# Performance work log

Hardware: AMD Instinct MI355X
Metric: run time of the kernel (lower is better)

The kernel has to match this reference:

```python
import jax, jax.numpy as jnp
import numpy as np
import jax.scipy.linalg

BATCH = 1048576
M_NUM = 2
DT = 0.0166667
NN_RATIO = 0.5
SLOPE = 0.01  # torch LeakyReLU default negative_slope


def setup_inputs() -> dict:
    key = jax.random.key(0)
    ks = jax.random.split(key, 16)
    inp = {}
    inp["SS"] = jax.random.normal(ks[0], (BATCH, 2), dtype=jnp.float32)
    inp["Alphas"] = jax.random.uniform(ks[1], (BATCH, M_NUM), dtype=jnp.float32)
    # per-muscle scalar parameters (positive so sqrt(K*I) is valid)
    inp["K0s"] = jax.random.uniform(ks[2], (M_NUM,), minval=0.5, maxval=1.5)
    inp["K1s"] = jax.random.uniform(ks[3], (M_NUM,), minval=0.5, maxval=1.5)
    inp["L0s"] = jax.random.uniform(ks[4], (M_NUM,), minval=0.5, maxval=1.5)
    inp["L1s"] = jax.random.uniform(ks[5], (M_NUM,), minval=0.1, maxval=0.6)
    inp["Ms"] = jnp.array([1.0, -1.0], dtype=jnp.float32)  # moment arms
    inp["I_p"] = jnp.array([1.0], dtype=jnp.float32)
    inp["B_p"] = jnp.array([0.05], dtype=jnp.float32)
    inp["K_p"] = jnp.array([1.0], dtype=jnp.float32)
    # per-muscle compensational MLP weights: 3-32-32-32-1 (eval mode, dropout off)
    s = 0.1
    inp["W1"] = jax.random.normal(ks[6], (M_NUM, 3, 32)) * s
    inp["b1"] = jax.random.normal(ks[7], (M_NUM, 32)) * s
    inp["W2"] = jax.random.normal(ks[8], (M_NUM, 32, 32)) * s
    inp["b2"] = jax.random.normal(ks[9], (M_NUM, 32)) * s
    inp["W3"] = jax.random.normal(ks[10], (M_NUM, 32, 32)) * s
    inp["b3"] = jax.random.normal(ks[11], (M_NUM, 32)) * s
    inp["W4"] = jax.random.normal(ks[12], (M_NUM, 32, 1)) * s
    inp["b4"] = jax.random.normal(ks[13], (M_NUM, 1)) * s
    return inp


def _leaky(x):
    return jnp.where(x >= 0, x, SLOPE * x)


def reference(SS, Alphas, K0s, K1s, L0s, L1s, Ms, I_p, B_p, K_p,
              W1, b1, W2, b2, W3, b3, W4, b4):
    B = SS.shape[0]
    a = jnp.clip(Alphas, 0.0, 1.0)                      # (B, m)
    # muscle length / speed via scalar moment arms
    l = SS[:, 0:1] * Ms[None, :]                        # (B, m)
    dl = SS[:, 1:2] * Ms[None, :]                       # (B, m)
    # compensational MLPs, vectorized over muscles
    x = jnp.stack([l, dl, a], axis=-1)                  # (B, m, 3)
    h = _leaky(jnp.einsum('bmi,mio->bmo', x, W1) + b1[None])
    h = _leaky(jnp.einsum('bmi,mio->bmo', h, W2) + b2[None])
    h = _leaky(jnp.einsum('bmi,mio->bmo', h, W3) + b3[None])
    nn_out = jnp.tanh(jnp.einsum('bmi,mio->bmo', h, W4) + b4[None])[..., 0] * NN_RATIO  # (B, m)

    I0, B0p, K0p = I_p[0], B_p[0], K_p[0]
    K_m = K0s[None, :] + K1s[None, :] * a               # (B, m)
    K_tot = jnp.sum(K_m * Ms[None, :] ** 2, axis=1)     # (B,)
    A10 = -(K_tot + K0p) / I0
    D = 2.0 * jnp.sqrt(K_tot * I0)
    A11 = -(D + B0p) / I0
    B_F = K_m * (L0s[None, :] + L1s[None, :] * a - jnp.abs(l)) \
        + K1s[None, :] * L1s[None, :] * a * a * nn_out   # (B, m)
    B10 = jnp.sum(B_F * Ms[None, :], axis=1) / I0       # (B,)

    # Build block matrix M6 = [[A*dt, B*dt, 0], [0, 0, I2], [0, 0, 0]]
    M6 = jnp.zeros((B, 6, 6), dtype=SS.dtype)
    M6 = M6.at[:, 0, 1].set(DT)
    M6 = M6.at[:, 1, 0].set(A10 * DT)
    M6 = M6.at[:, 1, 1].set(A11 * DT)
    M6 = M6.at[:, 1, 2].set(B10 * DT)
    M6 = M6.at[:, 1, 3].set(DT / I0)
    M6 = M6.at[:, 2, 4].set(1.0)
    M6 = M6.at[:, 3, 5].set(1.0)

    expMT = jax.vmap(jax.scipy.linalg.expm)(M6)         # (B, 6, 6)
    Ad = expMT[:, :2, :2]
    Bd1 = expMT[:, :2, 4:6]
    Bd0 = expMT[:, :2, 2:4] - Bd1
    u = jnp.array([1.0, 0.0], dtype=SS.dtype)           # U0 = U1 = [1, 0]
    SSout = (jnp.einsum('bij,bj->bi', Ad, SS)
             + jnp.einsum('bij,j->bi', Bd0, u)
             + jnp.einsum('bij,j->bi', Bd1, u))          # (B, 2)
    return SSout[:, :1], SSout
```

## Files before the change

### kernel.cpp

```cpp
#include <hip/hip_runtime.h>
#include <hip/hip_bf16.h>

#define NTHREADS 512
#define WAVES    8
#define NBLOCKS  768
#define DT_F     0.0166667f

typedef _Float16 f16x4 __attribute__((ext_vector_type(4)));
typedef _Float16 f16x2 __attribute__((ext_vector_type(2)));
typedef float    f32x4 __attribute__((ext_vector_type(4)));

#define BF16_PROBE 0xBF803F80u

#define OW1 0
#define OB1 192
#define OW2 256
#define OB2 2368
#define OW3 2432
#define OB3 4544
#define OW4 4608
#define OB4 4672
#define SMEM_F 4680

__device__ __forceinline__ float leaky(float x) { return fmaxf(x, 0.01f * x); }

__device__ __forceinline__ float tanh_fast(float x) {
    const float xc = fminf(fmaxf(x, -10.0f), 10.0f);
    const float t  = __expf(2.0f * xc);
    return (t - 1.0f) * __builtin_amdgcn_rcpf(t + 1.0f);
}

__device__ __forceinline__ f16x2 pkrtz(float a, float b) {
    return __builtin_bit_cast(f16x2, __builtin_amdgcn_cvt_pkrtz(a, b));
}

__device__ __forceinline__ f16x4 leaky_cvt(const f32x4 D) {
    f16x2 lo = pkrtz(D[0], D[1]);
    f16x2 hi = pkrtz(D[2], D[3]);
    const f16x2 sl = {(_Float16)0.01f, (_Float16)0.01f};
    lo = __builtin_elementwise_max(lo, lo * sl);
    hi = __builtin_elementwise_max(hi, hi * sl);
    return __builtin_shufflevector(lo, hi, 0, 1, 2, 3);
}

__device__ __forceinline__ void epilogue_math(
    const float* P, float ss0, float ss1, float a0, float a1,
    float nn0, float nn1, float& o0f, float& o1f)
{
    const float K00 = P[0], K01 = P[1], K10 = P[2], K11 = P[3];
    const float L00 = P[4], L01 = P[5], L10 = P[6], L11 = P[7];
    const float Ms0 = P[8], Ms1 = P[9];
    const float I0  = P[10], B0p = P[11], K0p = P[12];

    const float Km0   = fmaf(K10, a0, K00);
    const float Km1   = fmaf(K11, a1, K01);
    const float K_tot = Km0*Ms0*Ms0 + Km1*Ms1*Ms1;
    const float invI  = 1.0f / I0;
    const float A10   = -(K_tot + K0p) * invI;
    const float Dd    = 2.0f * sqrtf(K_tot * I0);
    const float A11   = -(Dd + B0p) * invI;
    const float absl0 = fabsf(ss0 * Ms0);
    const float absl1 = fabsf(ss0 * Ms1);
    const float BF0   = Km0 * (L00 + L10*a0 - absl0) + K10*L10*a0*a0*nn0;
    const float BF1   = Km1 * (L01 + L11*a1 - absl1) + K11*L11*a1*a1*nn1;
    const float B10   = (BF0*Ms0 + BF1*Ms1) * invI;

    const float t01 = DT_F;
    const float t10 = A10 * DT_F;
    const float t11 = A11 * DT_F;

    float p00 = 1.0f/120.0f, p01 = 0.0f, p10 = 0.0f, p11 = 1.0f/120.0f;
    const float coef[4] = {1.0f/24.0f, 1.0f/6.0f, 0.5f, 1.0f};
    #pragma unroll
    for (int j = 0; j < 4; ++j) {
        const float cj  = coef[j];
        const float n00 = p01*t10 + cj;
        const float n01 = p00*t01 + p01*t11;
        const float n10 = p11*t10;
        const float n11 = p10*t01 + p11*t11 + cj;
        p00 = n00; p01 = n01; p10 = n10; p11 = n11;
    }
    const float e00 = 1.0f + t01*p10;
    const float e01 = t01*p11;
    const float e10 = t10*p00 + t11*p10;
    const float e11 = 1.0f + t10*p01 + t11*p11;

    const float cscale = DT_F * B10;
    o0f = fmaf(e00, ss0, fmaf(e01, ss1, p01 * cscale));
    o1f = fmaf(e10, ss0, fmaf(e11, ss1, p11 * cscale));
}

__device__ __forceinline__ float ldb(const __hip_bfloat16* p, int i) {
    return __bfloat162float(p[i]);
}

__device__ void run_bf16_fallback(
    const void* SSv, const void* ALv, const void* K0sv, const void* K1sv,
    const void* L0sv, const void* L1sv, const void* Msv, const void* I_pv,
    const void* B_pv, const void* K_pv, const void* W1v, const void* b1v,
    const void* W2v, const void* b2v, const void* W3v, const void* b3v,
    const void* W4v, const void* b4v, void* outv, int batch)
{
    const __hip_bfloat16* SS = (const __hip_bfloat16*)SSv;
    const __hip_bfloat16* AL = (const __hip_bfloat16*)ALv;
    const __hip_bfloat16* W1 = (const __hip_bfloat16*)W1v;
    const __hip_bfloat16* b1 = (const __hip_bfloat16*)b1v;
    const __hip_bfloat16* W2 = (const __hip_bfloat16*)W2v;
    const __hip_bfloat16* b2 = (const __hip_bfloat16*)b2v;
    const __hip_bfloat16* W3 = (const __hip_bfloat16*)W3v;
    const __hip_bfloat16* b3 = (const __hip_bfloat16*)b3v;
    const __hip_bfloat16* W4 = (const __hip_bfloat16*)W4v;
    const __hip_bfloat16* b4 = (const __hip_bfloat16*)b4v;

    float P[13];
    P[0] = ldb((const __hip_bfloat16*)K0sv, 0); P[1] = ldb((const __hip_bfloat16*)K0sv, 1);
    P[2] = ldb((const __hip_bfloat16*)K1sv, 0); P[3] = ldb((const __hip_bfloat16*)K1sv, 1);
    P[4] = ldb((const __hip_bfloat16*)L0sv, 0); P[5] = ldb((const __hip_bfloat16*)L0sv, 1);
    P[6] = ldb((const __hip_bfloat16*)L1sv, 0); P[7] = ldb((const __hip_bfloat16*)L1sv, 1);
    P[8] = ldb((const __hip_bfloat16*)Msv, 0);  P[9] = ldb((const __hip_bfloat16*)Msv, 1);
    P[10] = ldb((const __hip_bfloat16*)I_pv, 0);
    P[11] = ldb((const __hip_bfloat16*)B_pv, 0);
    P[12] = ldb((const __hip_bfloat16*)K_pv, 0);

    const int stride = gridDim.x * blockDim.x;
    for (int e = blockIdx.x * blockDim.x + threadIdx.x; e < batch; e += stride) {
        const float ss0 = ldb(SS, 2*e), ss1 = ldb(SS, 2*e+1);
        float a0 = fminf(fmaxf(ldb(AL, 2*e),   0.0f), 1.0f);
        float a1 = fminf(fmaxf(ldb(AL, 2*e+1), 0.0f), 1.0f);
        float nn[2];
        #pragma unroll 1
        for (int m = 0; m < 2; ++m) {
            const float am = m ? a1 : a0;
            const float l = ss0 * P[8+m], dl = ss1 * P[8+m];
            float h[32];
            #pragma unroll
            for (int o = 0; o < 32; ++o)
                h[o] = leaky(fmaf(l, ldb(W1, m*96+o),
                             fmaf(dl, ldb(W1, m*96+32+o),
                             fmaf(am, ldb(W1, m*96+64+o), ldb(b1, m*32+o)))));
            float g[32];
            #pragma unroll 1
            for (int oc = 0; oc < 4; ++oc) {
                float acc[8];
                #pragma unroll
                for (int j = 0; j < 8; ++j) acc[j] = ldb(b2, m*32+oc*8+j);
                #pragma unroll
                for (int k = 0; k < 32; ++k) {
                    #pragma unroll
                    for (int j = 0; j < 8; ++j)
                        acc[j] = fmaf(h[k], ldb(W2, m*1024+k*32+oc*8+j), acc[j]);
                }
                #pragma unroll
                for (int j = 0; j < 8; ++j) g[oc*8+j] = leaky(acc[j]);
            }
            float h3[32];
            #pragma unroll 1
            for (int oc = 0; oc < 4; ++oc) {
                float acc[8];
                #pragma unroll
                for (int j = 0; j < 8; ++j) acc[j] = ldb(b3, m*32+oc*8+j);
                #pragma unroll
                for (int k = 0; k < 32; ++k) {
                    #pragma unroll
                    for (int j = 0; j < 8; ++j)
                        acc[j] = fmaf(g[k], ldb(W3, m*1024+k*32+oc*8+j), acc[j]);
                }
                #pragma unroll
                for (int j = 0; j < 8; ++j) h3[oc*8+j] = leaky(acc[j]);
            }
            float acc = ldb(b4, m);
            #pragma unroll
            for (int k = 0; k < 32; ++k) acc = fmaf(h3[k], ldb(W4, m*32+k), acc);
            nn[m] = tanh_fast(acc) * 0.5f;
        }
        float o0f, o1f;
        epilogue_math(P, ss0, ss1, a0, a1, nn[0], nn[1], o0f, o1f);
        __hip_bfloat16* out0 = (__hip_bfloat16*)outv;
        __hip_bfloat162* out1 = (__hip_bfloat162*)(out0 + batch);
        out0[e] = __float2bfloat16(o0f);
        __hip_bfloat162 pr;
        pr.x = __float2bfloat16(o0f);
        pr.y = __float2bfloat16(o1f);
        out1[e] = pr;
    }
}

__global__ __launch_bounds__(NTHREADS) void joint_kernel(
    const void* __restrict__ SSv, const void* __restrict__ ALv,
    const void* __restrict__ K0sv, const void* __restrict__ K1sv,
    const void* __restrict__ L0sv, const void* __restrict__ L1sv,
    const void* __restrict__ Msv,  const void* __restrict__ I_pv,
    const void* __restrict__ B_pv, const void* __restrict__ K_pv,
    const void* __restrict__ W1v,  const void* __restrict__ b1v,
    const void* __restrict__ W2v,  const void* __restrict__ b2v,
    const void* __restrict__ W3v,  const void* __restrict__ b3v,
    const void* __restrict__ W4v,  const void* __restrict__ b4v,
    void* __restrict__ outv, int batch)
{
    const unsigned probe = *(const unsigned*)Msv;
    if (probe == BF16_PROBE) {
        run_bf16_fallback(SSv, ALv, K0sv, K1sv, L0sv, L1sv, Msv, I_pv, B_pv,
                          K_pv, W1v, b1v, W2v, b2v, W3v, b3v, W4v, b4v,
                          outv, batch);
        return;
    }

    const float* SS = (const float*)SSv;
    const float* AL = (const float*)ALv;
    const float* W1 = (const float*)W1v;  const float* b1 = (const float*)b1v;
    const float* W2 = (const float*)W2v;  const float* b2 = (const float*)b2v;
    const float* W3 = (const float*)W3v;  const float* b3 = (const float*)b3v;
    const float* W4 = (const float*)W4v;  const float* b4 = (const float*)b4v;

    const int tid  = threadIdx.x;
    const int wave = tid >> 6;
    const int lane = tid & 63;
    const int n    = lane & 15;
    const int q    = lane >> 4;

    __shared__ __align__(16) float sm[SMEM_F];
    for (int i = tid; i < 192;  i += NTHREADS) sm[OW1+i] = W1[i];
    for (int i = tid; i < 2048; i += NTHREADS) {
        const int mi = i >> 10, rem = i & 1023, in = rem >> 5, out = rem & 31;
        sm[OW2 + mi*1056 + in*33 + out] = W2[i];
        sm[OW3 + mi*1056 + in*33 + out] = W3[i];
    }
    for (int i = tid; i < 64;   i += NTHREADS) {
        sm[OB1+i] = b1[i]; sm[OB2+i] = b2[i];
        sm[OB3+i] = b3[i]; sm[OW4+i] = W4[i];
    }
    if (tid < 2) sm[OB4+tid] = b4[tid];
    __syncthreads();

    f16x4 A1[2][2];
    #pragma unroll
    for (int mi = 0; mi < 2; ++mi)
        #pragma unroll
        for (int i = 0; i < 2; ++i)
            #pragma unroll
            for (int j = 0; j < 4; ++j) {
                const int k = q*4 + j;
                float v = 0.0f;
                if (k < 3)       v = sm[OW1 + mi*96 + k*32 + i*16 + n];
                else if (k == 3) v = sm[OB1 + mi*32 + i*16 + n];
                A1[mi][i][j] = (_Float16)v;
            }
    f16x4 A2[2][2][2], A3[2][2][2];
    #pragma unroll
    for (int mi = 0; mi < 2; ++mi)
        #pragma unroll
        for (int i = 0; i < 2; ++i)
            #pragma unroll
            for (int kb = 0; kb < 2; ++kb)
                #pragma unroll
                for (int j = 0; j < 4; ++j) {
                    const int in = kb*16 + q*4 + j;
                    A2[mi][i][kb][j] = (_Float16)sm[OW2 + mi*1056 + in*33 + i*16 + n];
                    A3[mi][i][kb][j] = (_Float16)sm[OW3 + mi*1056 + in*33 + i*16 + n];
                }
    f16x4 A4[2][2];
    #pragma unroll
    for (int mi = 0; mi < 2; ++mi)
        #pragma unroll
        for (int kb = 0; kb < 2; ++kb)
            #pragma unroll
            for (int j = 0; j < 4; ++j)
                A4[mi][kb][j] = (_Float16)sm[OW4 + mi*32 + kb*16 + q*4 + j];
    f32x4 Cb2[2][2], Cb3[2][2];
    #pragma unroll
    for (int mi = 0; mi < 2; ++mi) {
        #pragma unroll
        for (int i = 0; i < 2; ++i) {
            Cb2[mi][i] = *(const f32x4*)&sm[OB2 + mi*32 + i*16 + q*4];
            Cb3[mi][i] = *(const f32x4*)&sm[OB3 + mi*32 + i*16 + q*4];
        }
    }
    const float b4s0 = sm[OB4], b4s1 = sm[OB4+1];

    float P[13];
    P[0]  = ((const float*)K0sv)[0]; P[1]  = ((const float*)K0sv)[1];
    P[2]  = ((const float*)K1sv)[0]; P[3]  = ((const float*)K1sv)[1];
    P[4]  = ((const float*)L0sv)[0]; P[5]  = ((const float*)L0sv)[1];
    P[6]  = ((const float*)L1sv)[0]; P[7]  = ((const float*)L1sv)[1];
    P[8]  = ((const float*)Msv)[0];  P[9]  = ((const float*)Msv)[1];
    P[10] = ((const float*)I_pv)[0];
    P[11] = ((const float*)B_pv)[0];
    P[12] = ((const float*)K_pv)[0];

    const f32x4 zero = {0.0f, 0.0f, 0.0f, 0.0f};
    const int nGroups    = (batch + 63) >> 6;
    const int waveId     = blockIdx.x * WAVES + wave;
    const int waveStride = gridDim.x * WAVES;

    #pragma unroll 1
    for (int grp = waveId; grp < nGroups; grp += waveStride) {
        const int ebase = grp * 64;
        float my_r0 = 0.0f, my_r1 = 0.0f;

        #pragma unroll 1
        for (int p = 0; p < 2; ++p) {
            float2 s[2];
            float a0c[2], a1c[2];
            #pragma unroll
            for (int ti = 0; ti < 2; ++ti) {
                const int e  = ebase + (2*p + ti)*16 + n;
                const int eg = min(e, batch - 1);
                s[ti] = ((const float2*)SS)[eg];
                const float2 al = ((const float2*)AL)[eg];
                a0c[ti] = fminf(fmaxf(al.x, 0.0f), 1.0f);
                a1c[ti] = fminf(fmaxf(al.y, 0.0f), 1.0f);
            }

            f16x4 B1[2][2];
            #pragma unroll
            for (int ti = 0; ti < 2; ++ti)
                #pragma unroll
                for (int mi = 0; mi < 2; ++mi) {
                    const float Msm = P[8 + mi];
                    const float am  = mi ? a1c[ti] : a0c[ti];
                    const f16x2 blo = pkrtz(s[ti].x * Msm, s[ti].y * Msm);
                    const f16x2 bhi = pkrtz(am, 1.0f);
                    B1[ti][mi] = __builtin_shufflevector(blo, bhi, 0, 1, 2, 3);
                }

            f32x4 D[2][2][2];
            #pragma unroll
            for (int ti = 0; ti < 2; ++ti)
                #pragma unroll
                for (int mi = 0; mi < 2; ++mi) {
                    D[ti][mi][0] = __builtin_amdgcn_mfma_f32_16x16x16f16(A1[mi][0], B1[ti][mi], zero, 0, 0, 0);
                    D[ti][mi][1] = __builtin_amdgcn_mfma_f32_16x16x16f16(A1[mi][1], B1[ti][mi], zero, 0, 0, 0);
                }
            f16x4 Bx[2][2][2];
            #pragma unroll
            for (int ti = 0; ti < 2; ++ti)
                #pragma unroll
                for (int mi = 0; mi < 2; ++mi) {
                    Bx[ti][mi][0] = leaky_cvt(D[ti][mi][0]);
                    Bx[ti][mi][1] = leaky_cvt(D[ti][mi][1]);
                }

            #pragma unroll
            for (int ti = 0; ti < 2; ++ti)
                #pragma unroll
                for (int mi = 0; mi < 2; ++mi) {
                    D[ti][mi][0] = __builtin_amdgcn_mfma_f32_16x16x16f16(A2[mi][0][1], Bx[ti][mi][1],
                                   __builtin_amdgcn_mfma_f32_16x16x16f16(A2[mi][0][0], Bx[ti][mi][0],
                                       Cb2[mi][0], 0, 0, 0), 0, 0, 0);
                    D[ti][mi][1] = __builtin_amdgcn_mfma_f32_16x16x16f16(A2[mi][1][1], Bx[ti][mi][1],
                                   __builtin_amdgcn_mfma_f32_16x16x16f16(A2[mi][1][0], Bx[ti][mi][0],
                                       Cb2[mi][1], 0, 0, 0), 0, 0, 0);
                }
            #pragma unroll
            for (int ti = 0; ti < 2; ++ti)
                #pragma unroll
                for (int mi = 0; mi < 2; ++mi) {
                    Bx[ti][mi][0] = leaky_cvt(D[ti][mi][0]);
                    Bx[ti][mi][1] = leaky_cvt(D[ti][mi][1]);
                }

            #pragma unroll
            for (int ti = 0; ti < 2; ++ti)
                #pragma unroll
                for (int mi = 0; mi < 2; ++mi) {
                    D[ti][mi][0] = __builtin_amdgcn_mfma_f32_16x16x16f16(A3[mi][0][1], Bx[ti][mi][1],
                                   __builtin_amdgcn_mfma_f32_16x16x16f16(A3[mi][0][0], Bx[ti][mi][0],
                                       Cb3[mi][0], 0, 0, 0), 0, 0, 0);
                    D[ti][mi][1] = __builtin_amdgcn_mfma_f32_16x16x16f16(A3[mi][1][1], Bx[ti][mi][1],
                                   __builtin_amdgcn_mfma_f32_16x16x16f16(A3[mi][1][0], Bx[ti][mi][0],
                                       Cb3[mi][1], 0, 0, 0), 0, 0, 0);
                }
            #pragma unroll
            for (int ti = 0; ti < 2; ++ti)
                #pragma unroll
                for (int mi = 0; mi < 2; ++mi) {
                    Bx[ti][mi][0] = leaky_cvt(D[ti][mi][0]);
                    Bx[ti][mi][1] = leaky_cvt(D[ti][mi][1]);
                }

            #pragma unroll
            for (int ti = 0; ti < 2; ++ti) {
                const bool own = (q == (2*p + ti));
                #pragma unroll
                for (int mi = 0; mi < 2; ++mi) {
                    f32x4 G = __builtin_amdgcn_mfma_f32_16x16x16f16(A4[mi][1], Bx[ti][mi][1],
                              __builtin_amdgcn_mfma_f32_16x16x16f16(A4[mi][0], Bx[ti][mi][0],
                                  zero, 0, 0, 0), 0, 0, 0);
                    const float r = G[0] + (mi ? b4s1 : b4s0);
                    if (mi == 0) my_r0 = own ? r : my_r0;
                    else         my_r1 = own ? r : my_r1;
                }
            }
        }

        const int eo  = ebase + lane;
        const int eog = min(eo, batch - 1);
        const float2 se  = ((const float2*)SS)[eog];
        const float2 ale = ((const float2*)AL)[eog];
        const float a0 = fminf(fmaxf(ale.x, 0.0f), 1.0f);
        const float a1 = fminf(fmaxf(ale.y, 0.0f), 1.0f);
        const float nn0 = tanh_fast(my_r0) * 0.5f;
        const float nn1 = tanh_fast(my_r1) * 0.5f;
        float o0f, o1f;
        epilogue_math(P, se.x, se.y, a0, a1, nn0, nn1, o0f, o1f);
        if (eo < batch) {
            ((float*)outv)[eo] = o0f;
            ((float2*)((float*)outv + batch))[eo] = make_float2(o0f, o1f);
        }
    }
}

extern "C" void kernel_launch(void* const* d_in, const int* in_sizes, int n_in,
                              void* d_out, int out_size, void* d_ws, size_t ws_size,
                              hipStream_t stream) {
    const int batch = in_sizes[0] / 2;
    const int nGroups = (batch + 63) >> 6;
    int grid = NBLOCKS;
    const int maxBlocks = (nGroups + WAVES - 1) / WAVES;
    if (grid > maxBlocks) grid = maxBlocks;
    joint_kernel<<<grid, NTHREADS, 0, stream>>>(
        d_in[0], d_in[1], d_in[2], d_in[3], d_in[4], d_in[5], d_in[6],
        d_in[7], d_in[8], d_in[9], d_in[10], d_in[11], d_in[12], d_in[13],
        d_in[14], d_in[15], d_in[16], d_in[17], d_out, batch);
}
```

Measured before the change: 129.0 us.

## Use 16x16x32 f16 MFMA with permuted hidden layout and fixed-work blocks

Replaces pairs of chained 16x16x16 MFMAs for the 32-wide hidden layers with single 16x16x32 MFMAs. The output-neuron mapping of layer weights is permuted (gh0) so that each lane's leaky-converted D outputs concatenate directly into the 8-element B operand of the next layer. This halves the MFMA instruction count and shortens the dependent accumulation chains. It also drops the persistent grid-stride loop in favor of 256-thread blocks that each process a fixed 4 groups per wave. That launches many more blocks, so the shared-memory weight staging is repeated more often. Tail blocks rely on clamped indices and the eo<batch guard.

Measured after the change: 126.8 us. No clear change (-1.7%).

```diff
diff --git a/kernel.cpp b/kernel.cpp
--- a/kernel.cpp
+++ b/kernel.cpp
@@ -1,11 +1,12 @@
 #include <hip/hip_runtime.h>
 #include <hip/hip_bf16.h>
 
-#define NTHREADS 512
-#define WAVES    8
-#define NBLOCKS  768
+#define NTHREADS 256
+#define WAVES    4
+#define GPW      4
 #define DT_F     0.0166667f
 
+typedef _Float16 f16x8 __attribute__((ext_vector_type(8)));
 typedef _Float16 f16x4 __attribute__((ext_vector_type(4)));
 typedef _Float16 f16x2 __attribute__((ext_vector_type(2)));
 typedef float    f32x4 __attribute__((ext_vector_type(4)));
@@ -41,6 +42,10 @@
     lo = __builtin_elementwise_max(lo, lo * sl);
     hi = __builtin_elementwise_max(hi, hi * sl);
     return __builtin_shufflevector(lo, hi, 0, 1, 2, 3);
+}
+
+__device__ __forceinline__ f16x8 concat8(const f16x4 a, const f16x4 b) {
+    return __builtin_shufflevector(a, b, 0, 1, 2, 3, 4, 5, 6, 7);
 }
 
 __device__ __forceinline__ void epilogue_math(
@@ -217,6 +222,7 @@
     const int lane = tid & 63;
     const int n    = lane & 15;
     const int q    = lane >> 4;
+    const int gh0  = ((n >> 2) << 3) + (n & 3);
 
     __shared__ __align__(16) float sm[SMEM_F];
     for (int i = tid; i < 192;  i += NTHREADS) sm[OW1+i] = W1[i];
@@ -236,45 +242,43 @@
     #pragma unroll
     for (int mi = 0; mi < 2; ++mi)
         #pragma unroll
-        for (int i = 0; i < 2; ++i)
+        for (int h = 0; h < 2; ++h)
             #pragma unroll
             for (int j = 0; j < 4; ++j) {
                 const int k = q*4 + j;
+                const int g = gh0 + h*4;
                 float v = 0.0f;
-                if (k < 3)       v = sm[OW1 + mi*96 + k*32 + i*16 + n];
-                else if (k == 3) v = sm[OB1 + mi*32 + i*16 + n];
-                A1[mi][i][j] = (_Float16)v;
-            }
-    f16x4 A2[2][2][2], A3[2][2][2];
+                if (k < 3)       v = sm[OW1 + mi*96 + k*32 + g];
+                else if (k == 3) v = sm[OB1 + mi*32 + g];
+                A1[mi][h][j] = (_Float16)v;
+            }
+    f16x8 A2[2][2], A3[2][2];
     #pragma unroll
     for (int mi = 0; mi < 2; ++mi)
         #pragma unroll
-        for (int i = 0; i < 2; ++i)
-            #pragma unroll
-            for (int kb = 0; kb < 2; ++kb)
-                #pragma unroll
-                for (int j = 0; j < 4; ++j) {
-                    const int in = kb*16 + q*4 + j;
-                    A2[mi][i][kb][j] = (_Float16)sm[OW2 + mi*1056 + in*33 + i*16 + n];
-                    A3[mi][i][kb][j] = (_Float16)sm[OW3 + mi*1056 + in*33 + i*16 + n];
-                }
-    f16x4 A4[2][2];
+        for (int h = 0; h < 2; ++h) {
+            const int g = gh0 + h*4;
+            #pragma unroll
+            for (int j = 0; j < 8; ++j) {
+                const int in = q*8 + j;
+                A2[mi][h][j] = (_Float16)sm[OW2 + mi*1056 + in*33 + g];
+                A3[mi][h][j] = (_Float16)sm[OW3 + mi*1056 + in*33 + g];
+            }
+        }
+    f16x8 A4[2];
     #pragma unroll
     for (int mi = 0; mi < 2; ++mi)
         #pragma unroll
-        for (int kb = 0; kb < 2; ++kb)
-            #pragma unroll
-            for (int j = 0; j < 4; ++j)
-                A4[mi][kb][j] = (_Float16)sm[OW4 + mi*32 + kb*16 + q*4 + j];
+        for (int j = 0; j < 8; ++j)
+            A4[mi][j] = (_Float16)sm[OW4 + mi*32 + q*8 + j];
     f32x4 Cb2[2][2], Cb3[2][2];
     #pragma unroll
-    for (int mi = 0; mi < 2; ++mi) {
+    for (int mi = 0; mi < 2; ++mi)
         #pragma unroll
-        for (int i = 0; i < 2; ++i) {
-            Cb2[mi][i] = *(const f32x4*)&sm[OB2 + mi*32 + i*16 + q*4];
-            Cb3[mi][i] = *(const f32x4*)&sm[OB3 + mi*32 + i*16 + q*4];
+        for (int h = 0; h < 2; ++h) {
+            Cb2[mi][h] = *(const f32x4*)&sm[OB2 + mi*32 + q*8 + h*4];
+            Cb3[mi][h] = *(const f32x4*)&sm[OB3 + mi*32 + q*8 + h*4];
         }
-    }
     const float b4s0 = sm[OB4], b4s1 = sm[OB4+1];
 
     float P[13];
@@ -288,13 +292,11 @@
     P[12] = ((const float*)K_pv)[0];
 
     const f32x4 zero = {0.0f, 0.0f, 0.0f, 0.0f};
-    const int nGroups    = (batch + 63) >> 6;
-    const int waveId     = blockIdx.x * WAVES + wave;
-    const int waveStride = gridDim.x * WAVES;
+    const int groupBase = (blockIdx.x * WAVES + wave) * GPW;
 
     #pragma unroll 1
-    for (int grp = waveId; grp < nGroups; grp += waveStride) {
-        const int ebase = grp * 64;
+    for (int g = 0; g < GPW; ++g) {
+        const int ebase = (groupBase + g) * 64;
         float my_r0 = 0.0f, my_r1 = 0.0f;
 
         #pragma unroll 1
@@ -331,61 +333,45 @@
                     D[ti][mi][0] = __builtin_amdgcn_mfma_f32_16x16x16f16(A1[mi][0], B1[ti][mi], zero, 0, 0, 0);
                     D[ti][mi][1] = __builtin_amdgcn_mfma_f32_16x16x16f16(A1[mi][1], B1[ti][mi], zero, 0, 0, 0);
                 }
-            f16x4 Bx[2][2][2];
+            f16x8 Bx[2][2];
+            #pragma unroll
+            for (int ti = 0; ti < 2; ++ti)
+                #pragma unroll
+                for (int mi = 0; mi < 2; ++mi)
+                    Bx[ti][mi] = concat8(leaky_cvt(D[ti][mi][0]), leaky_cvt(D[ti][mi][1]));
+
             #pragma unroll
             for (int ti = 0; ti < 2; ++ti)
                 #pragma unroll
                 for (int mi = 0; mi < 2; ++mi) {
-                    Bx[ti][mi][0] = leaky_cvt(D[ti][mi][0]);
-                    Bx[ti][mi][1] = leaky_cvt(D[ti][mi][1]);
-                }
+                    D[ti][mi][0] = __builtin_amdgcn_mfma_f32_16x16x32_f16(A2[mi][0], Bx[ti][mi], Cb2[mi][0], 0, 0, 0);
+                    D[ti][mi][1] = __builtin_amdgcn_mfma_f32_16x16x32_f16(A2[mi][1], Bx[ti][mi], Cb2[mi][1], 0, 0, 0);
+                }
+            #pragma unroll
+            for (int ti = 0; ti < 2; ++ti)
+                #pragma unroll
+                for (int mi = 0; mi < 2; ++mi)
+                    Bx[ti][mi] = concat8(leaky_cvt(D[ti][mi][0]), leaky_cvt(D[ti][mi][1]));
 
             #pragma unroll
             for (int ti = 0; ti < 2; ++ti)
                 #pragma unroll
                 for (int mi = 0; mi < 2; ++mi) {
-                    D[ti][mi][0] = __builtin_amdgcn_mfma_f32_16x16x16f16(A2[mi][0][1], Bx[ti][mi][1],
-                                   __builtin_amdgcn_mfma_f32_16x16x16f16(A2[mi][0][0], Bx[ti][mi][0],
-                                       Cb2[mi][0], 0, 0, 0), 0, 0, 0);
-                    D[ti][mi][1] = __builtin_amdgcn_mfma_f32_16x16x16f16(A2[mi][1][1], Bx[ti][mi][1],
-                                   __builtin_amdgcn_mfma_f32_16x16x16f16(A2[mi][1][0], Bx[ti][mi][0],
-                                       Cb2[mi][1], 0, 0, 0), 0, 0, 0);
-                }
-            #pragma unroll
-            for (int ti = 0; ti < 2; ++ti)
-                #pragma unroll
-                for (int mi = 0; mi < 2; ++mi) {
-                    Bx[ti][mi][0] = leaky_cvt(D[ti][mi][0]);
-                    Bx[ti][mi][1] = leaky_cvt(D[ti][mi][1]);
-                }
-
-            #pragma unroll
-            for (int ti = 0; ti < 2; ++ti)
-                #pragma unroll
-                for (int mi = 0; mi < 2; ++mi) {
-                    D[ti][mi][0] = __builtin_amdgcn_mfma_f32_16x16x16f16(A3[mi][0][1], Bx[ti][mi][1],
-                                   __builtin_amdgcn_mfma_f32_16x16x16f16(A3[mi][0][0], Bx[ti][mi][0],
-                                       Cb3[mi][0], 0, 0, 0), 0, 0, 0);
-                    D[ti][mi][1] = __builtin_amdgcn_mfma_f32_16x16x16f16(A3[mi][1][1], Bx[ti][mi][1],
-                                   __builtin_amdgcn_mfma_f32_16x16x16f16(A3[mi][1][0], Bx[ti][mi][0],
-                                       Cb3[mi][1], 0, 0, 0), 0, 0, 0);
-                }
-            #pragma unroll
-            for (int ti = 0; ti < 2; ++ti)
-                #pragma unroll
-                for (int mi = 0; mi < 2; ++mi) {
-                    Bx[ti][mi][0] = leaky_cvt(D[ti][mi][0]);
-                    Bx[ti][mi][1] = leaky_cvt(D[ti][mi][1]);
-                }
+                    D[ti][mi][0] = __builtin_amdgcn_mfma_f32_16x16x32_f16(A3[mi][0], Bx[ti][mi], Cb3[mi][0], 0, 0, 0);
+                    D[ti][mi][1] = __builtin_amdgcn_mfma_f32_16x16x32_f16(A3[mi][1], Bx[ti][mi], Cb3[mi][1], 0, 0, 0);
+                }
+            #pragma unroll
+            for (int ti = 0; ti < 2; ++ti)
+                #pragma unroll
+                for (int mi = 0; mi < 2; ++mi)
+                    Bx[ti][mi] = concat8(leaky_cvt(D[ti][mi][0]), leaky_cvt(D[ti][mi][1]));
 
             #pragma unroll
             for (int ti = 0; ti < 2; ++ti) {
                 const bool own = (q == (2*p + ti));
                 #pragma unroll
                 for (int mi = 0; mi < 2; ++mi) {
-                    f32x4 G = __builtin_amdgcn_mfma_f32_16x16x16f16(A4[mi][1], Bx[ti][mi][1],
-                              __builtin_amdgcn_mfma_f32_16x16x16f16(A4[mi][0], Bx[ti][mi][0],
-                                  zero, 0, 0, 0), 0, 0, 0);
+                    f32x4 G = __builtin_amdgcn_mfma_f32_16x16x32_f16(A4[mi], Bx[ti][mi], zero, 0, 0, 0);
                     const float r = G[0] + (mi ? b4s1 : b4s0);
                     if (mi == 0) my_r0 = own ? r : my_r0;
                     else         my_r1 = own ? r : my_r1;
@@ -414,10 +400,8 @@
                               void* d_out, int out_size, void* d_ws, size_t ws_size,
                               hipStream_t stream) {
     const int batch = in_sizes[0] / 2;
-    const int nGroups = (batch + 63) >> 6;
-    int grid = NBLOCKS;
-    const int maxBlocks = (nGroups + WAVES - 1) / WAVES;
-    if (grid > maxBlocks) grid = maxBlocks;
+    const int elemsPerBlock = 64 * GPW * WAVES;
+    const int grid = (batch + elemsPerBlock - 1) / elemsPerBlock;
     joint_kernel<<<grid, NTHREADS, 0, stream>>>(
         d_in[0], d_in[1], d_in[2], d_in[3], d_in[4], d_in[5], d_in[6],
         d_in[7], d_in[8], d_in[9], d_in[10], d_in[11], d_in[12], d_in[13],
```
